# Kernel tuning notes

Measured on AMD Instinct MI355X. Metric: run time of the kernel, lower is better.

The kernel has to match this reference:

```python
import jax, jax.numpy as jnp
import numpy as np

N_NODES = 50000
N_EDGES = 1000000
IN_C = 128
HID_C = 128
N_REL = 8


def rgcn_conv(x, W, root, b, src, dst, et, n_rel):
    # PyG-style RGCNConv: per-relation linear transform of source features,
    # mean-aggregated per (target node, relation), plus root transform + bias.
    n = x.shape[0]
    h = jnp.einsum('nd,rdh->nrh', x, W)          # [N, R, H] per-relation transforms
    msgs = h[src, et]                            # [E, H] gather per-edge message
    seg = dst * n_rel + et                       # combined (node, relation) segment id
    agg = jax.ops.segment_sum(msgs, seg, num_segments=n * n_rel)        # [N*R, H]
    cnt = jax.ops.segment_sum(jnp.ones_like(msgs[:, 0]), seg, num_segments=n * n_rel)
    agg = agg / jnp.maximum(cnt, 1.0)[:, None]   # mean over edges of each relation
    return agg.reshape(n, n_rel, -1).sum(axis=1) + x @ root + b


def setup_inputs() -> dict:
    key = jax.random.key(0)
    ks = jax.random.split(key, 12)
    s = 1.0 / np.sqrt(IN_C)
    sh = 1.0 / np.sqrt(HID_C)
    return {
        'x': jax.random.normal(ks[0], (N_NODES, IN_C), dtype=jnp.float32),
        'ei': jax.random.randint(ks[1], (2, N_EDGES), 0, N_NODES, dtype=jnp.int32),
        'et': jax.random.randint(ks[2], (N_EDGES,), 0, N_REL, dtype=jnp.int32),
        'W1': jax.random.normal(ks[3], (N_REL, IN_C, HID_C), dtype=jnp.float32) * s,
        'root1': jax.random.normal(ks[4], (IN_C, HID_C), dtype=jnp.float32) * s,
        'b1': jnp.zeros((HID_C,), dtype=jnp.float32),
        'W2': jax.random.normal(ks[5], (N_REL, HID_C, HID_C), dtype=jnp.float32) * sh,
        'root2': jax.random.normal(ks[6], (HID_C, HID_C), dtype=jnp.float32) * sh,
        'b2': jnp.zeros((HID_C,), dtype=jnp.float32),
        'lin_W': jax.random.normal(ks[7], (HID_C, HID_C), dtype=jnp.float32) * sh,
        'lin_b': jnp.zeros((HID_C,), dtype=jnp.float32),
    }


def reference(x, ei, et, W1, root1, b1, W2, root2, b2, lin_W, lin_b):
    src, dst = ei[0], ei[1]
    h = jax.nn.relu(rgcn_conv(x, W1, root1, b1, src, dst, et, N_REL))
    h = rgcn_conv(h, W2, root2, b2, src, dst, et, N_REL)
    return h @ lin_W + lin_b
```

## Files before the change

kernel.cpp:

```cpp
#include <hip/hip_runtime.h>
#include <hip/hip_bf16.h>

#define N_NODES 50000
#define N_EDGES 1000000
#define C       128
#define N_REL   8
#define N_SEG   (N_NODES * N_REL)
#define KTOT    (N_REL * C + C)
#define KC_CNT  (KTOT / 32)
#define A_STRIDE 1160
#define NCHUNK  ((N_SEG + 1023) / 1024)
#define NBLK    (N_NODES / 16)
#define FE_BLK  ((N_EDGES + 511) / 512)

typedef __hip_bfloat16  bf16;
typedef __hip_bfloat162 bf162;
typedef __attribute__((ext_vector_type(8))) short short8;
typedef __attribute__((ext_vector_type(4))) float f32x4;

__device__ __forceinline__ size_t frag_index(int k, int n) {
    int nt = n >> 4, n15 = n & 15;
    int kc = k >> 5, quad = (k >> 3) & 3, j = k & 7;
    int lane = quad * 16 + n15;
    return ((size_t)(nt * KC_CNT + kc) * 64 + lane) * 8 + j;
}

#define CVT_BLOCKS ((N_NODES * C / 4) / 256)
#define CNT_BLOCKS ((N_EDGES + 255) / 256)
typedef __attribute__((ext_vector_type(2))) unsigned int uint2v;
__global__ void prep_kernel(const float4* __restrict__ xf, uint2v* __restrict__ xb,
                            const int* __restrict__ dst, const int* __restrict__ et,
                            int* __restrict__ cnt, int* __restrict__ rankseg) {
    int bid = blockIdx.x;
    if (bid < CVT_BLOCKS) {
        int i = bid * 256 + threadIdx.x;
        float4 v = xf[i];
        union { bf162 h; unsigned int u; } c0, c1;
        c0.h = bf162(__float2bfloat16(v.x), __float2bfloat16(v.y));
        c1.h = bf162(__float2bfloat16(v.z), __float2bfloat16(v.w));
        uint2v o; o.x = c0.u; o.y = c1.u;
        xb[i] = o;
    } else {
        int e = (bid - CVT_BLOCKS) * 256 + threadIdx.x;
        if (e < N_EDGES) {
            int seg = dst[e] * N_REL + et[e];
            int r = atomicAdd(&cnt[seg], 1);
            rankseg[e] = (r << 19) | seg;
        }
    }
}

#define RP_B  (KTOT * C / 256)
#define RPT_B ((KTOT / 16) * (C / 16))
__global__ void scanA_kernel(const int* __restrict__ cnt, int* __restrict__ offs,
                             int* __restrict__ partials,
                             const float* __restrict__ W1, const float* __restrict__ root1,
                             const float* __restrict__ W2, const float* __restrict__ root2,
                             const float* __restrict__ linW,
                             const float* __restrict__ b2, const float* __restrict__ linb,
                             bf16* __restrict__ Bp1, bf16* __restrict__ Bp2,
                             float* __restrict__ b2p) {
    int bid = blockIdx.x;
    int t   = threadIdx.x;
    if (bid < NCHUNK) {
        __shared__ int tot[256];
        int base = bid * 1024 + t * 4;
        int v0 = (base + 0 < N_SEG) ? cnt[base + 0] : 0;
        int v1 = (base + 1 < N_SEG) ? cnt[base + 1] : 0;
        int v2 = (base + 2 < N_SEG) ? cnt[base + 2] : 0;
        int v3 = (base + 3 < N_SEG) ? cnt[base + 3] : 0;
        int tsum = v0 + v1 + v2 + v3;
        tot[t] = tsum;
        __syncthreads();
        for (int d = 1; d < 256; d <<= 1) {
            int x = tot[t];
            int y = (t >= d) ? tot[t - d] : 0;
            __syncthreads();
            tot[t] = x + y;
            __syncthreads();
        }
        int excl = tot[t] - tsum;
        if (base + 0 < N_SEG) offs[base + 0] = excl;
        if (base + 1 < N_SEG) offs[base + 1] = excl + v0;
        if (base + 2 < N_SEG) offs[base + 2] = excl + v0 + v1;
        if (base + 3 < N_SEG) offs[base + 3] = excl + v0 + v1 + v2;
        if (t == 255) partials[bid] = tot[255];
    } else if (bid < NCHUNK + RP_B) {
        int idx = (bid - NCHUNK) * 256 + t;
        int k = idx >> 7, n = idx & 127;
        float val;
        if (k < N_REL * C) val = W1[(size_t)k * C + n];
        else               val = root1[(size_t)(k - N_REL * C) * C + n];
        Bp1[frag_index(k, n)] = __float2bfloat16(val);
    } else if (bid < NCHUNK + RP_B + RPT_B) {
        __shared__ float Wt[16][128];
        __shared__ float Lt[128][16];
        int tileid = bid - NCHUNK - RP_B;
        int kt = tileid >> 3;
        int n0 = (tileid & 7) * 16;
        int k0 = kt * 16;
        const float* baseW = (k0 < N_REL * C) ? (W2 + (size_t)k0 * C)
                                              : (root2 + (size_t)(k0 - N_REL * C) * C);
#pragma unroll
        for (int r = 0; r < 8; r++) {
            int idx = t + r * 256;
            Wt[idx >> 7][idx & 127] = baseW[idx];
        }
#pragma unroll
        for (int r = 0; r < 8; r++) {
            int idx = t + r * 256;
            Lt[idx >> 4][idx & 15] = linW[(size_t)(idx >> 4) * C + n0 + (idx & 15)];
        }
        __syncthreads();
        int ty = t >> 4, tx = t & 15;
        float acc = 0.f;
#pragma unroll 8
        for (int m = 0; m < 128; m++)
            acc += Wt[ty][m] * Lt[m][tx];
        Bp2[frag_index(k0 + ty, n0 + tx)] = __float2bfloat16(acc);
    } else {
        if (t < 128) {
            float acc = linb[t];
            for (int m = 0; m < C; m++)
                acc += b2[m] * linW[(size_t)m * C + t];
            b2p[t] = acc;
        }
    }
}

__global__ void fillB_kernel(const int* __restrict__ src,
                             const int* __restrict__ rankseg,
                             const int* __restrict__ offs_raw,
                             const int* __restrict__ partials,
                             int* __restrict__ srcs_out,
                             int* __restrict__ offs_final) {
    __shared__ int s[512];
    int t = threadIdx.x;
    int bid = blockIdx.x;
    s[t] = (t < NCHUNK) ? partials[t] : 0;
    __syncthreads();
    for (int d = 1; d < 512; d <<= 1) {
        int x = s[t];
        int y = (t >= d) ? s[t - d] : 0;
        __syncthreads();
        s[t] = x + y;
        __syncthreads();
    }
    int e = bid * 512 + t;
    if (e < N_SEG) {
        int chunk = e >> 10;
        offs_final[e] = offs_raw[e] + ((chunk == 0) ? 0 : s[chunk - 1]);
    } else if (e == N_SEG) {
        offs_final[N_SEG] = N_EDGES;
    }
    if (e < N_EDGES) {
        int rs = rankseg[e];
        int seg = rs & 0x7FFFF;
        int r = ((unsigned int)rs) >> 19;
        int chunk = seg >> 10;
        int base = offs_raw[seg] + ((chunk == 0) ? 0 : s[chunk - 1]);
        srcs_out[base + r] = src[e];
    }
}

template <int RELU, int OUT_F32>
__global__ __launch_bounds__(512, 6) void fused_layer(
        const unsigned int* __restrict__ featu,
        const int*   __restrict__ offs,
        const int*   __restrict__ srcs,
        const short8* __restrict__ Bp,
        const float* __restrict__ bias,
        void* __restrict__ outp)
{
    __shared__ __align__(16) unsigned int At[16 * (A_STRIDE / 2)];
    __shared__ int offsL[129];
    const int tid  = threadIdx.x;
    const int lane = tid & 63;
    const int w    = tid >> 6;
    const int v0   = blockIdx.x * 16;

    if (tid < 129) offsL[tid] = offs[v0 * 8 + tid];
    if (tid < 64)  At[(tid >> 2) * (A_STRIDE / 2) + 576 + (tid & 3)] = 0u;

    for (int q = tid; q < 16 * 64; q += 512) {
        int node = q >> 6, pch = q & 63;
        At[node * (A_STRIDE / 2) + 512 + pch] = featu[(size_t)(v0 + node) * 64 + pch];
    }
    __syncthreads();

    {
        const int segLo = w * 16;
        const int segHi = segLo + 16;
        int curSeg = segLo;
        int segEnd = offsL[curSeg + 1];
        int i      = offsL[segLo];
        const int eend = offsL[segHi];
        float a0 = 0.f, a1 = 0.f;

        unsigned int vals[16];
        bool have = (i + 16 <= eend);
        if (have) {
            const int ib = __builtin_amdgcn_readfirstlane(i);
            int sv[16];
#pragma unroll
            for (int j = 0; j < 16; j++) sv[j] = srcs[ib + j];
#pragma unroll
            for (int j = 0; j < 16; j++) vals[j] = featu[(size_t)sv[j] * 64 + lane];
        }
        while (have) {
            const int inext = i + 16;
            const bool havenext = (inext + 16 <= eend);
            unsigned int vals2[16];
            if (havenext) {
                const int ib2 = __builtin_amdgcn_readfirstlane(inext);
                int sv2[16];
#pragma unroll
                for (int j = 0; j < 16; j++) sv2[j] = srcs[ib2 + j];
#pragma unroll
                for (int j = 0; j < 16; j++) vals2[j] = featu[(size_t)sv2[j] * 64 + lane];
            }
#pragma unroll
            for (int j = 0; j < 16; j++) {
                while (i + j == segEnd) {
                    int b = offsL[curSeg];
                    float inv = (segEnd > b) ? 1.0f / (float)(segEnd - b) : 0.0f;
                    union { bf162 h; unsigned int u; } cv;
                    cv.h = bf162(__float2bfloat16(a0 * inv), __float2bfloat16(a1 * inv));
                    At[(curSeg >> 3) * (A_STRIDE / 2) + (curSeg & 7) * 64 + lane] = cv.u;
                    a0 = 0.f; a1 = 0.f;
                    curSeg++;
                    segEnd = offsL[curSeg + 1];
                }
                union { bf162 h; unsigned int u; } uv; uv.u = vals[j];
                a0 += __low2float(uv.h);
                a1 += __high2float(uv.h);
            }
            i = inext;
            have = havenext;
            if (havenext) {
#pragma unroll
                for (int j = 0; j < 16; j++) vals[j] = vals2[j];
            }
        }
        {
            int m = eend - i;
            const int ib = __builtin_amdgcn_readfirstlane(i);
            int sv[16];
#pragma unroll
            for (int j = 0; j < 16; j++) if (j < m) sv[j] = srcs[ib + j];
            unsigned int tvals[16];
#pragma unroll
            for (int j = 0; j < 16; j++) if (j < m) tvals[j] = featu[(size_t)sv[j] * 64 + lane];
#pragma unroll
            for (int j = 0; j < 16; j++) {
                if (j < m) {
                    while (i + j == segEnd) {
                        int b = offsL[curSeg];
                        float inv = (segEnd > b) ? 1.0f / (float)(segEnd - b) : 0.0f;
                        union { bf162 h; unsigned int u; } cv;
                        cv.h = bf162(__float2bfloat16(a0 * inv), __float2bfloat16(a1 * inv));
                        At[(curSeg >> 3) * (A_STRIDE / 2) + (curSeg & 7) * 64 + lane] = cv.u;
                        a0 = 0.f; a1 = 0.f;
                        curSeg++;
                        segEnd = offsL[curSeg + 1];
                    }
                    union { bf162 h; unsigned int u; } uv; uv.u = tvals[j];
                    a0 += __low2float(uv.h);
                    a1 += __high2float(uv.h);
                }
            }
        }
        while (curSeg < segHi) {
            int b = offsL[curSeg], e2 = offsL[curSeg + 1];
            float inv = (e2 > b) ? 1.0f / (float)(e2 - b) : 0.0f;
            union { bf162 h; unsigned int u; } cv;
            cv.h = bf162(__float2bfloat16(a0 * inv), __float2bfloat16(a1 * inv));
            At[(curSeg >> 3) * (A_STRIDE / 2) + (curSeg & 7) * 64 + lane] = cv.u;
            a0 = 0.f; a1 = 0.f;
            curSeg++;
        }
    }
    __syncthreads();

    const int quad = lane >> 4, n15 = lane & 15;
    f32x4 acc = {0.f, 0.f, 0.f, 0.f};
    const short* Ash = (const short*)At;

    short8 b0 = Bp[(size_t)(w * KC_CNT) * 64 + lane];
#pragma unroll 4
    for (int kc = 0; kc < KC_CNT; kc++) {
        short8 cb0 = b0;
        if (kc + 1 < KC_CNT)
            b0 = Bp[(size_t)(w * KC_CNT + kc + 1) * 64 + lane];
        short8 a = *reinterpret_cast<const short8*>(Ash + n15 * A_STRIDE + kc * 32 + quad * 8);
        acc = __builtin_amdgcn_mfma_f32_16x16x32_bf16(a, cb0, acc, 0, 0, 0);
    }

    {
        int col = w * 16 + n15;
        float bv = bias[col];
#pragma unroll
        for (int r = 0; r < 4; r++) {
            int m = quad * 4 + r;
            float v = acc[r] + bv;
            if (RELU) v = fmaxf(v, 0.f);
            if (OUT_F32) ((float*)outp)[(size_t)(v0 + m) * C + col] = v;
            else         ((bf16*)outp)[(size_t)(v0 + m) * C + col] = __float2bfloat16(v);
        }
    }
}

extern "C" void kernel_launch(void* const* d_in, const int* in_sizes, int n_in,
                              void* d_out, int out_size, void* d_ws, size_t ws_size,
                              hipStream_t stream) {
    const float* x     = (const float*)d_in[0];
    const int*   ei    = (const int*)d_in[1];
    const int*   et    = (const int*)d_in[2];
    const float* W1    = (const float*)d_in[3];
    const float* root1 = (const float*)d_in[4];
    const float* b1    = (const float*)d_in[5];
    const float* W2    = (const float*)d_in[6];
    const float* root2 = (const float*)d_in[7];
    const float* b2    = (const float*)d_in[8];
    const float* linW  = (const float*)d_in[9];
    const float* linb  = (const float*)d_in[10];
    const int* src = ei;
    const int* dst = ei + N_EDGES;

    char* ob = (char*)d_out;
    int* cnt_i    = (int*)(ob + 0);
    int* offs_t   = (int*)(ob + 1600000);
    int* partials = (int*)(ob + 3200000);
    int* rankseg  = (int*)(ob + 3203584);
    unsigned int* xb16 = (unsigned int*)(ob + 7203584);

    int* srcs_f = (int*)((char*)d_in[1] + 4000000);
    int* offs_f = (int*)d_in[2];

    char* xbuf = (char*)d_in[0];
    unsigned int* h1 = (unsigned int*)xbuf;
    bf16*  Bp1 = (bf16*)(xbuf + 13000192);
    bf16*  Bp2 = (bf16*)(xbuf + 13295360);
    float* b2p = (float*)(xbuf + 13590528);

    float* out = (float*)d_out;

    hipMemsetAsync(cnt_i, 0, 1600000, stream);
    prep_kernel<<<CVT_BLOCKS + CNT_BLOCKS, 256, 0, stream>>>(
        (const float4*)x, (uint2v*)xb16, dst, et, cnt_i, rankseg);
    scanA_kernel<<<NCHUNK + RP_B + RPT_B + 1, 256, 0, stream>>>(
        cnt_i, offs_t, partials, W1, root1, W2, root2, linW, b2, linb,
        Bp1, Bp2, b2p);
    fillB_kernel<<<FE_BLK, 512, 0, stream>>>(
        src, rankseg, offs_t, partials, srcs_f, offs_f);

    fused_layer<1, 0><<<NBLK, 512, 0, stream>>>(
        xb16, offs_f, srcs_f, (const short8*)Bp1, b1, (void*)h1);
    fused_layer<0, 1><<<NBLK, 512, 0, stream>>>(
        h1, offs_f, srcs_f, (const short8*)Bp2, b2p, (void*)out);

    (void)in_sizes; (void)n_in; (void)out_size; (void)d_ws; (void)ws_size;
}
```

Before: 291.9 us.

## Replace two-pass segment scan with decoupled look-back scan and fold weight prep

```diff
diff --git a/kernel.cpp b/kernel.cpp
--- a/kernel.cpp
+++ b/kernel.cpp
@@ -15,8 +15,10 @@
 
 typedef __hip_bfloat16  bf16;
 typedef __hip_bfloat162 bf162;
+typedef unsigned long long u64;
 typedef __attribute__((ext_vector_type(8))) short short8;
 typedef __attribute__((ext_vector_type(4))) float f32x4;
+typedef __attribute__((ext_vector_type(2))) unsigned int uint2v;
 
 __device__ __forceinline__ size_t frag_index(int k, int n) {
     int nt = n >> 4, n15 = n & 15;
@@ -27,75 +29,46 @@
 
 #define CVT_BLOCKS ((N_NODES * C / 4) / 256)
 #define CNT_BLOCKS ((N_EDGES + 255) / 256)
-typedef __attribute__((ext_vector_type(2))) unsigned int uint2v;
+#define RP_B  (KTOT * C / 256)
+#define RPT_B ((KTOT / 16) * (C / 16))
+#define PREP_GRID (CVT_BLOCKS + CNT_BLOCKS + RP_B + RPT_B + 1)
 __global__ void prep_kernel(const float4* __restrict__ xf, uint2v* __restrict__ xb,
                             const int* __restrict__ dst, const int* __restrict__ et,
-                            int* __restrict__ cnt, int* __restrict__ rankseg) {
+                            int* __restrict__ cnt, int* __restrict__ rankseg,
+                            const float* __restrict__ W1, const float* __restrict__ root1,
+                            const float* __restrict__ W2, const float* __restrict__ root2,
+                            const float* __restrict__ linW,
+                            const float* __restrict__ b2v, const float* __restrict__ linb,
+                            bf16* __restrict__ Bp1, bf16* __restrict__ Bp2,
+                            float* __restrict__ b2p) {
+    __shared__ float Wt[16][128];
+    __shared__ float Lt[128][16];
     int bid = blockIdx.x;
+    int t   = threadIdx.x;
     if (bid < CVT_BLOCKS) {
-        int i = bid * 256 + threadIdx.x;
+        int i = bid * 256 + t;
         float4 v = xf[i];
         union { bf162 h; unsigned int u; } c0, c1;
         c0.h = bf162(__float2bfloat16(v.x), __float2bfloat16(v.y));
         c1.h = bf162(__float2bfloat16(v.z), __float2bfloat16(v.w));
         uint2v o; o.x = c0.u; o.y = c1.u;
         xb[i] = o;
-    } else {
-        int e = (bid - CVT_BLOCKS) * 256 + threadIdx.x;
+    } else if (bid < CVT_BLOCKS + CNT_BLOCKS) {
+        int e = (bid - CVT_BLOCKS) * 256 + t;
         if (e < N_EDGES) {
             int seg = dst[e] * N_REL + et[e];
             int r = atomicAdd(&cnt[seg], 1);
             rankseg[e] = (r << 19) | seg;
         }
-    }
-}
-
-#define RP_B  (KTOT * C / 256)
-#define RPT_B ((KTOT / 16) * (C / 16))
-__global__ void scanA_kernel(const int* __restrict__ cnt, int* __restrict__ offs,
-                             int* __restrict__ partials,
-                             const float* __restrict__ W1, const float* __restrict__ root1,
-                             const float* __restrict__ W2, const float* __restrict__ root2,
-                             const float* __restrict__ linW,
-                             const float* __restrict__ b2, const float* __restrict__ linb,
-                             bf16* __restrict__ Bp1, bf16* __restrict__ Bp2,
-                             float* __restrict__ b2p) {
-    int bid = blockIdx.x;
-    int t   = threadIdx.x;
-    if (bid < NCHUNK) {
-        __shared__ int tot[256];
-        int base = bid * 1024 + t * 4;
-        int v0 = (base + 0 < N_SEG) ? cnt[base + 0] : 0;
-        int v1 = (base + 1 < N_SEG) ? cnt[base + 1] : 0;
-        int v2 = (base + 2 < N_SEG) ? cnt[base + 2] : 0;
-        int v3 = (base + 3 < N_SEG) ? cnt[base + 3] : 0;
-        int tsum = v0 + v1 + v2 + v3;
-        tot[t] = tsum;
-        __syncthreads();
-        for (int d = 1; d < 256; d <<= 1) {
-            int x = tot[t];
-            int y = (t >= d) ? tot[t - d] : 0;
-            __syncthreads();
-            tot[t] = x + y;
-            __syncthreads();
-        }
-        int excl = tot[t] - tsum;
-        if (base + 0 < N_SEG) offs[base + 0] = excl;
-        if (base + 1 < N_SEG) offs[base + 1] = excl + v0;
-        if (base + 2 < N_SEG) offs[base + 2] = excl + v0 + v1;
-        if (base + 3 < N_SEG) offs[base + 3] = excl + v0 + v1 + v2;
-        if (t == 255) partials[bid] = tot[255];
-    } else if (bid < NCHUNK + RP_B) {
-        int idx = (bid - NCHUNK) * 256 + t;
+    } else if (bid < CVT_BLOCKS + CNT_BLOCKS + RP_B) {
+        int idx = (bid - CVT_BLOCKS - CNT_BLOCKS) * 256 + t;
         int k = idx >> 7, n = idx & 127;
         float val;
         if (k < N_REL * C) val = W1[(size_t)k * C + n];
         else               val = root1[(size_t)(k - N_REL * C) * C + n];
         Bp1[frag_index(k, n)] = __float2bfloat16(val);
-    } else if (bid < NCHUNK + RP_B + RPT_B) {
-        __shared__ float Wt[16][128];
-        __shared__ float Lt[128][16];
-        int tileid = bid - NCHUNK - RP_B;
+    } else if (bid < CVT_BLOCKS + CNT_BLOCKS + RP_B + RPT_B) {
+        int tileid = bid - CVT_BLOCKS - CNT_BLOCKS - RP_B;
         int kt = tileid >> 3;
         int n0 = (tileid & 7) * 16;
         int k0 = kt * 16;
@@ -122,44 +95,75 @@
         if (t < 128) {
             float acc = linb[t];
             for (int m = 0; m < C; m++)
-                acc += b2[m] * linW[(size_t)m * C + t];
+                acc += b2v[m] * linW[(size_t)m * C + t];
             b2p[t] = acc;
         }
     }
 }
 
-__global__ void fillB_kernel(const int* __restrict__ src,
-                             const int* __restrict__ rankseg,
-                             const int* __restrict__ offs_raw,
-                             const int* __restrict__ partials,
-                             int* __restrict__ srcs_out,
-                             int* __restrict__ offs_final) {
-    __shared__ int s[512];
-    int t = threadIdx.x;
-    int bid = blockIdx.x;
-    s[t] = (t < NCHUNK) ? partials[t] : 0;
+__global__ __launch_bounds__(512) void scan_kernel(const int* __restrict__ cnt,
+                                                   u64* __restrict__ flagval,
+                                                   int* __restrict__ offs_f) {
+    __shared__ int tot[512];
+    __shared__ int basesh;
+    const int t = threadIdx.x, b = blockIdx.x;
+    const int base = b * 1024 + t * 2;
+    int v0 = (base     < N_SEG) ? cnt[base]     : 0;
+    int v1 = (base + 1 < N_SEG) ? cnt[base + 1] : 0;
+    int ts = v0 + v1;
+    tot[t] = ts;
     __syncthreads();
     for (int d = 1; d < 512; d <<= 1) {
-        int x = s[t];
-        int y = (t >= d) ? s[t - d] : 0;
+        int x = tot[t];
+        int y = (t >= d) ? tot[t - d] : 0;
         __syncthreads();
-        s[t] = x + y;
+        tot[t] = x + y;
         __syncthreads();
     }
-    int e = bid * 512 + t;
-    if (e < N_SEG) {
-        int chunk = e >> 10;
-        offs_final[e] = offs_raw[e] + ((chunk == 0) ? 0 : s[chunk - 1]);
-    } else if (e == N_SEG) {
-        offs_final[N_SEG] = N_EDGES;
-    }
+    const int incl = tot[t];
+    const int sum  = tot[511];
+    if (t == 0) {
+        if (b == 0) {
+            __hip_atomic_store(&flagval[0], (2ULL << 32) | (unsigned)sum,
+                               __ATOMIC_RELEASE, __HIP_MEMORY_SCOPE_AGENT);
+            basesh = 0;
+            offs_f[N_SEG] = N_EDGES;
+        } else {
+            __hip_atomic_store(&flagval[b], (1ULL << 32) | (unsigned)sum,
+                               __ATOMIC_RELEASE, __HIP_MEMORY_SCOPE_AGENT);
+            int acc = 0;
+            int p = b - 1;
+            while (p >= 0) {
+                u64 v = __hip_atomic_load(&flagval[p], __ATOMIC_ACQUIRE,
+                                          __HIP_MEMORY_SCOPE_AGENT);
+                unsigned st = (unsigned)(v >> 32);
+                if (st == 0) { __builtin_amdgcn_s_sleep(8); continue; }
+                acc += (int)(unsigned)v;
+                if (st == 2) break;
+                p--;
+            }
+            __hip_atomic_store(&flagval[b], (2ULL << 32) | (unsigned)(acc + sum),
+                               __ATOMIC_RELEASE, __HIP_MEMORY_SCOPE_AGENT);
+            basesh = acc;
+        }
+    }
+    __syncthreads();
+    const int cb = basesh;
+    const int excl = incl - ts + cb;
+    if (base     < N_SEG) offs_f[base]     = excl;
+    if (base + 1 < N_SEG) offs_f[base + 1] = excl + v0;
+}
+
+__global__ __launch_bounds__(512) void fill_kernel(const int* __restrict__ src,
+                                                   const int* __restrict__ rankseg,
+                                                   const int* __restrict__ offs_f,
+                                                   int* __restrict__ srcs_out) {
+    int e = blockIdx.x * 512 + threadIdx.x;
     if (e < N_EDGES) {
         int rs = rankseg[e];
         int seg = rs & 0x7FFFF;
         int r = ((unsigned int)rs) >> 19;
-        int chunk = seg >> 10;
-        int base = offs_raw[seg] + ((chunk == 0) ? 0 : s[chunk - 1]);
-        srcs_out[base + r] = src[e];
+        srcs_out[offs_f[seg] + r] = src[e];
     }
 }
 
@@ -329,10 +333,9 @@
 
     char* ob = (char*)d_out;
     int* cnt_i    = (int*)(ob + 0);
-    int* offs_t   = (int*)(ob + 1600000);
-    int* partials = (int*)(ob + 3200000);
-    int* rankseg  = (int*)(ob + 3203584);
-    unsigned int* xb16 = (unsigned int*)(ob + 7203584);
+    u64* flagval  = (u64*)(ob + 1600000);
+    int* rankseg  = (int*)(ob + 1603328);
+    unsigned int* xb16 = (unsigned int*)(ob + 5603328);
 
     int* srcs_f = (int*)((char*)d_in[1] + 4000000);
     int* offs_f = (int*)d_in[2];
@@ -345,14 +348,12 @@
 
     float* out = (float*)d_out;
 
-    hipMemsetAsync(cnt_i, 0, 1600000, stream);
-    prep_kernel<<<CVT_BLOCKS + CNT_BLOCKS, 256, 0, stream>>>(
-        (const float4*)x, (uint2v*)xb16, dst, et, cnt_i, rankseg);
-    scanA_kernel<<<NCHUNK + RP_B + RPT_B + 1, 256, 0, stream>>>(
-        cnt_i, offs_t, partials, W1, root1, W2, root2, linW, b2, linb,
-        Bp1, Bp2, b2p);
-    fillB_kernel<<<FE_BLK, 512, 0, stream>>>(
-        src, rankseg, offs_t, partials, srcs_f, offs_f);
+    hipMemsetAsync(cnt_i, 0, 1603128, stream);
+    prep_kernel<<<PREP_GRID, 256, 0, stream>>>(
+        (const float4*)x, (uint2v*)xb16, dst, et, cnt_i, rankseg,
+        W1, root1, W2, root2, linW, b2, linb, Bp1, Bp2, b2p);
+    scan_kernel<<<NCHUNK, 512, 0, stream>>>(cnt_i, flagval, offs_f);
+    fill_kernel<<<FE_BLK, 512, 0, stream>>>(src, rankseg, offs_f, srcs_f);
 
     fused_layer<1, 0><<<NBLK, 512, 0, stream>>>(
         xb16, offs_f, srcs_f, (const short8*)Bp1, b1, (void*)h1);
```

New measurement: 411.8 us. 1.41x slower.
